# Optimization experiments

Hardware: AMD Instinct MI355X
Metric: run time of the kernel (lower is better)

The kernel has to match this reference:

```python
import math
import jax, jax.numpy as jnp
import numpy as np

GROUPS = 8

def setup_inputs() -> dict:
    key = jax.random.key(0)
    ks = jax.random.split(key, 6)
    N, H, W, C = 8, 128, 128, 512
    s = 1.0 / math.sqrt(C)
    return {
        "x": jax.random.normal(ks[0], (N, H, W, C), dtype=jnp.float32),
        "Wq": jax.random.normal(ks[1], (C, C), dtype=jnp.float32) * s,
        "Wk": jax.random.normal(ks[2], (C, C), dtype=jnp.float32) * s,
        "Wv": jax.random.normal(ks[3], (C, C), dtype=jnp.float32) * s,
        "Wo": jax.random.normal(ks[4], (C, C), dtype=jnp.float32) * s,
        "bo": jnp.zeros((C,), dtype=jnp.float32),
    }

def reference(x, Wq, Wk, Wv, Wo, bo):
    # width=False: attend along H axis -> permute to [N, W, H, C]
    x = jnp.transpose(x, (0, 2, 1, 3))
    N, W, H, C = x.shape
    g = GROUPS
    gp = C // g  # group_planes (head dim)
    xr = x.reshape(N * W, H, C)
    # torch nn.Linear: y = x @ W^T
    q = (xr @ Wq.T).reshape(N * W, H, g, gp)
    k = (xr @ Wk.T).reshape(N * W, H, g, gp)
    v = (xr @ Wv.T).reshape(N * W, H, g, gp)
    attn = jnp.einsum('nigc,njgc->nijg', q, k / math.sqrt(gp))
    attn = jax.nn.softmax(attn, axis=2)
    out = jnp.einsum('nijg,njgc->nigc', attn, v)
    out = out.reshape(N * W, H, C)
    out = out @ Wo.T + bo
    out = out.reshape(N, W, H, C)
    return jnp.transpose(out, (0, 2, 1, 3))
```

## Files before the change

kernel.cpp:

```cpp
#include <hip/hip_runtime.h>
#include <stdint.h>


#define QKV_LD 1536

typedef __attribute__((ext_vector_type(4))) float f32x4;
typedef __attribute__((ext_vector_type(8))) short bf16x8;
typedef unsigned short u16;
typedef unsigned int u32;

static __device__ __forceinline__ u16 f2bf(float f){
    union { float f; u32 u; } v; v.f = f;
    u32 r = v.u + 0x7fffu + ((v.u >> 16) & 1u);
    return (u16)(r >> 16);
}

static __device__ __forceinline__ void gload16(const void* g, void* l){
    __builtin_amdgcn_global_load_lds((const __attribute__((address_space(1))) void*)g,
                                     (__attribute__((address_space(3))) void*)l, 16, 0, 0);
}

__global__ void k_wconv(const float* __restrict__ Wq, const float* __restrict__ Wk,
                        const float* __restrict__ Wv, const float* __restrict__ Wo,
                        u16* __restrict__ Wcat, u16* __restrict__ Wob){
    int e = (blockIdx.x * 256 + threadIdx.x) * 4;
    if (e < 1536*512) {
        int row = e >> 9, col = e & 511;
        const float* s = (row < 512) ? (Wq + row*512)
                        : (row < 1024 ? Wk + (row-512)*512 : Wv + (row-1024)*512);
        float4 v = *(const float4*)(s + col);
        ushort4 o = { f2bf(v.x), f2bf(v.y), f2bf(v.z), f2bf(v.w) };
        *(ushort4*)(Wcat + e) = o;
    } else {
        int e2 = e - 1536*512;
        float4 v = *(const float4*)(Wo + e2);
        ushort4 o = { f2bf(v.x), f2bf(v.y), f2bf(v.z), f2bf(v.w) };
        *(ushort4*)(Wob + e2) = o;
    }
}

__global__ void k_xconv(const float* __restrict__ x, u16* __restrict__ xb, int n0){
    int t = blockIdx.x * 256 + threadIdx.x;
    int ml = t >> 6;
    int c0 = (t & 63) << 3;
    int nl = ml >> 7, h = ml & 127;
    int n = n0 + nl, nb = n >> 7, w = n & 127;
    const float* src = x + (size_t)((nb*128 + h)*128 + w) * 512 + c0;
    float4 a = *(const float4*)(src);
    float4 b = *(const float4*)(src + 4);
    uint4 o;
    o.x = (u32)f2bf(a.x) | ((u32)f2bf(a.y) << 16);
    o.y = (u32)f2bf(a.z) | ((u32)f2bf(a.w) << 16);
    o.z = (u32)f2bf(b.x) | ((u32)f2bf(b.y) << 16);
    o.w = (u32)f2bf(b.z) | ((u32)f2bf(b.w) << 16);
    *(uint4*)(xb + (size_t)ml*512 + c0) = o;
}

template<int LDA, int NCOL, bool OUTPROJ>
__global__ __launch_bounds__(256, 2) void k_gemm(const u16* __restrict__ A, const u16* __restrict__ B,
                                                 void* __restrict__ Cout, const float* __restrict__ bias,
                                                 int n0, int nrow){
    __shared__ char sm[32768];
    const int tid = threadIdx.x;
    const int wid = tid >> 6, lane = tid & 63, lg = lane >> 4, li = lane & 15;
    const int bid = blockIdx.x;
    const int xcd = bid & 7, l = bid >> 3;
    const int row_tile = xcd * (nrow >> 3) + l / NCOL;
    const int col_tile = l % NCOL;
    const int m0 = row_tile * 128, nn0 = col_tile * 128;
    const int wm = (wid >> 1) * 64, wn = (wid & 1) * 64;

    f32x4 acc[4][4];
    #pragma unroll
    for (int i = 0; i < 4; ++i)
        #pragma unroll
        for (int j = 0; j < 4; ++j)
            acc[i][j] = f32x4{0.f, 0.f, 0.f, 0.f};

    for (int k0 = 0; k0 < 512; k0 += 64) {
        if (k0) __syncthreads();
        #pragma unroll
        for (int it = 0; it < 4; ++it) {
            int gi = it*256 + tid;
            int row = gi >> 3, gs = gi & 7;
            int sw = (gs ^ (row & 7)) << 4;
            gload16((const char*)(A + (size_t)(m0 + row)*LDA + k0) + sw,
                    sm + it*4096 + wid*1024);
            gload16((const char*)(B + (size_t)(nn0 + row)*512 + k0) + sw,
                    sm + 16384 + it*4096 + wid*1024);
        }
        __syncthreads();
        #pragma unroll
        for (int ks = 0; ks < 2; ++ks) {
            bf16x8 af[4], bfr[4];
            #pragma unroll
            for (int t = 0; t < 4; ++t) {
                int ra = wm + t*16 + li;
                af[t]  = *(const bf16x8*)(sm + ra*128 + ((ks*64 + lg*16) ^ ((ra & 7) << 4)));
                int rb = wn + t*16 + li;
                bfr[t] = *(const bf16x8*)(sm + 16384 + rb*128 + ((ks*64 + lg*16) ^ ((rb & 7) << 4)));
            }
            #pragma unroll
            for (int i = 0; i < 4; ++i)
                #pragma unroll
                for (int j = 0; j < 4; ++j)
                    acc[i][j] = __builtin_amdgcn_mfma_f32_16x16x32_bf16(af[i], bfr[j], acc[i][j], 0, 0, 0);
        }
    }

    if (!OUTPROJ) {
        u16* C = (u16*)Cout;
        #pragma unroll
        for (int i = 0; i < 4; ++i)
            #pragma unroll
            for (int j = 0; j < 4; ++j)
                #pragma unroll
                for (int r = 0; r < 4; ++r) {
                    int row = m0 + wm + i*16 + lg*4 + r;
                    int col = nn0 + wn + j*16 + li;
                    C[(size_t)row*QKV_LD + col] = f2bf(acc[i][j][r]);
                }
    } else {
        float* C = (float*)Cout;
        #pragma unroll
        for (int i = 0; i < 4; ++i)
            #pragma unroll
            for (int j = 0; j < 4; ++j)
                #pragma unroll
                for (int r = 0; r < 4; ++r) {
                    int row = m0 + wm + i*16 + lg*4 + r;
                    int col = nn0 + wn + j*16 + li;
                    int mg = n0*128 + row;
                    int n = mg >> 7, ii = mg & 127;
                    int nb = n >> 7, w = n & 127;
                    C[(size_t)((nb*128 + ii)*128 + w) * 512 + col] = acc[i][j][r] + bias[col];
                }
    }
}

__global__ __launch_bounds__(256, 2) void k_attn(u16* __restrict__ QKV){
    __shared__ char sm[52224];
    const int g = blockIdx.x;
    const int nl = blockIdx.y;
    const int tid = threadIdx.x;
    const int wid = tid >> 6, lane = tid & 63, lg = lane >> 4, li = lane & 15;

    u16* Qg = QKV + (size_t)nl*128*QKV_LD + g*64;

    #pragma unroll
    for (int it = 0; it < 4; ++it) {
        int gi = it*256 + tid;
        int row = gi >> 3, gs = gi & 7;
        int sw = (gs ^ (row & 7)) << 4;
        gload16((const char*)(Qg + (size_t)row*QKV_LD) + sw,        sm + it*4096 + wid*1024);
        gload16((const char*)(Qg + 512 + (size_t)row*QKV_LD) + sw,  sm + 16384 + it*4096 + wid*1024);
    }
    {
        int j = tid & 127, ch = tid >> 7;
        const u16* src = Qg + 1024 + (size_t)j*QKV_LD + ch*32;
        uint4 a0 = *(const uint4*)(src);
        uint4 a1 = *(const uint4*)(src + 8);
        uint4 a2 = *(const uint4*)(src + 16);
        uint4 a3 = *(const uint4*)(src + 24);
        u32 w[16] = {a0.x,a0.y,a0.z,a0.w, a1.x,a1.y,a1.z,a1.w,
                     a2.x,a2.y,a2.z,a2.w, a3.x,a3.y,a3.z,a3.w};
        char* dst = sm + 34816 + ch*32*272 + j*2;
        #pragma unroll
        for (int cc = 0; cc < 32; ++cc) {
            u32 word = w[cc >> 1];
            u16 val = (cc & 1) ? (u16)(word >> 16) : (u16)(word & 0xffffu);
            *(u16*)(dst + cc*272) = val;
        }
    }
    __syncthreads();

    const int i0w = wid*32;
    f32x4 s[2][8];
    #pragma unroll
    for (int t = 0; t < 2; ++t)
        #pragma unroll
        for (int tj = 0; tj < 8; ++tj)
            s[t][tj] = f32x4{0.f,0.f,0.f,0.f};

    #pragma unroll
    for (int ks = 0; ks < 2; ++ks) {
        bf16x8 qf[2];
        #pragma unroll
        for (int t = 0; t < 2; ++t) {
            int ra = i0w + t*16 + li;
            qf[t] = *(const bf16x8*)(sm + ra*128 + ((ks*64 + lg*16) ^ ((ra & 7) << 4)));
        }
        #pragma unroll
        for (int tj = 0; tj < 8; ++tj) {
            int rb = tj*16 + li;
            bf16x8 kf = *(const bf16x8*)(sm + 16384 + rb*128 + ((ks*64 + lg*16) ^ ((rb & 7) << 4)));
            #pragma unroll
            for (int t = 0; t < 2; ++t)
                s[t][tj] = __builtin_amdgcn_mfma_f32_16x16x32_bf16(qf[t], kf, s[t][tj], 0, 0, 0);
        }
    }
    __syncthreads();

    char* pb = sm + wid*8704;
    #pragma unroll
    for (int t = 0; t < 2; ++t) {
        #pragma unroll
        for (int r = 0; r < 4; ++r) {
            float mx = -1e30f;
            #pragma unroll
            for (int tj = 0; tj < 8; ++tj) mx = fmaxf(mx, s[t][tj][r]);
            #pragma unroll
            for (int off = 1; off < 16; off <<= 1) mx = fmaxf(mx, __shfl_xor(mx, off, 64));
            float p[8]; float sum = 0.f;
            #pragma unroll
            for (int tj = 0; tj < 8; ++tj) { p[tj] = __expf((s[t][tj][r] - mx)*0.125f); sum += p[tj]; }
            #pragma unroll
            for (int off = 1; off < 16; off <<= 1) sum += __shfl_xor(sum, off, 64);
            float inv = 1.0f / sum;
            int prow = t*16 + lg*4 + r;
            #pragma unroll
            for (int tj = 0; tj < 8; ++tj)
                *(u16*)(pb + prow*272 + (tj*16 + li)*2) = f2bf(p[tj]*inv);
        }
    }

    f32x4 o[2][4];
    #pragma unroll
    for (int t = 0; t < 2; ++t)
        #pragma unroll
        for (int tc = 0; tc < 4; ++tc)
            o[t][tc] = f32x4{0.f,0.f,0.f,0.f};

    #pragma unroll
    for (int ks = 0; ks < 4; ++ks) {
        bf16x8 pf[2];
        #pragma unroll
        for (int t = 0; t < 2; ++t)
            pf[t] = *(const bf16x8*)(pb + (t*16 + li)*272 + (ks*64 + lg*16));
        #pragma unroll
        for (int tc = 0; tc < 4; ++tc) {
            bf16x8 vf = *(const bf16x8*)(sm + 34816 + (tc*16 + li)*272 + (ks*64 + lg*16));
            #pragma unroll
            for (int t = 0; t < 2; ++t)
                o[t][tc] = __builtin_amdgcn_mfma_f32_16x16x32_bf16(pf[t], vf, o[t][tc], 0, 0, 0);
        }
    }

    #pragma unroll
    for (int t = 0; t < 2; ++t)
        #pragma unroll
        for (int tc = 0; tc < 4; ++tc)
            #pragma unroll
            for (int r = 0; r < 4; ++r) {
                int irow = i0w + t*16 + lg*4 + r;
                int col = tc*16 + li;
                Qg[(size_t)irow*QKV_LD + col] = f2bf(o[t][tc][r]);
            }
}

extern "C" void kernel_launch(void* const* d_in, const int* in_sizes, int n_in,
                              void* d_out, int out_size, void* d_ws, size_t ws_size,
                              hipStream_t stream){
    const float* x  = (const float*)d_in[0];
    const float* Wq = (const float*)d_in[1];
    const float* Wk = (const float*)d_in[2];
    const float* Wv = (const float*)d_in[3];
    const float* Wo = (const float*)d_in[4];
    const float* bo = (const float*)d_in[5];

    char* ws = (char*)d_ws;
    u16* Wcat = (u16*)ws;
    u16* Wob  = Wcat + 1536*512;

    int CN = 1024;
    while (CN > 64 && (size_t)2097152 + (size_t)CN*524288 > ws_size) CN >>= 1;
    u16* xb  = (u16*)(ws + 2097152);
    u16* QKV = xb + (size_t)CN*128*512;

    k_wconv<<<1024, 256, 0, stream>>>(Wq, Wk, Wv, Wo, Wcat, Wob);
    int nch = 1024 / CN;
    for (int ch = 0; ch < nch; ++ch) {
        int n0 = ch * CN;
        k_xconv<<<CN*32, 256, 0, stream>>>(x, xb, n0);
        k_gemm<512,    12, false><<<CN*12, 256, 0, stream>>>(xb, Wcat, QKV, nullptr, 0, CN);
        k_attn<<<dim3(8, CN), 256, 0, stream>>>(QKV);
        k_gemm<QKV_LD, 4,  true ><<<CN*4,  256, 0, stream>>>(QKV, Wob, d_out, bo, n0, CN);
    }
}
```

Before: 663.1 us.

## Replace GEMM with 256x256-tile, 8-wave, double-buffered pipelined kernel

Swaps the 128x128 single-buffered GEMM for a 256x256 tile kernel with 8 waves, 128KB of dynamic LDS, and double-buffered global-to-LDS loads. Prefetch of the next k-slab is interleaved with MFMA phases using explicit vmcnt waits, barriers and setprio. The goal is to hide memory latency and raise data reuse per tile in both the QKV and output projections. In exchange it uses more LDS and registers and launches fewer, larger blocks, which may leave some CUs idle at tile boundaries.

Measured after the change: 626.3 us. 1.06x faster.

```diff
diff --git a/kernel.cpp b/kernel.cpp
--- a/kernel.cpp
+++ b/kernel.cpp
@@ -8,6 +8,11 @@
 typedef __attribute__((ext_vector_type(8))) short bf16x8;
 typedef unsigned short u16;
 typedef unsigned int u32;
+
+#define CBAR() asm volatile("" ::: "memory")
+#define SBAR() do { CBAR(); __builtin_amdgcn_s_barrier(); CBAR(); } while(0)
+#define LGKM0() do { asm volatile("s_waitcnt lgkmcnt(0)" ::: "memory"); __builtin_amdgcn_sched_barrier(0); } while(0)
+#define VMC(n) asm volatile("s_waitcnt vmcnt(" #n ")" ::: "memory")
 
 static __device__ __forceinline__ u16 f2bf(float f){
     union { float f; u32 u; } v; v.f = f;
@@ -57,83 +62,159 @@
 }
 
 template<int LDA, int NCOL, bool OUTPROJ>
-__global__ __launch_bounds__(256, 2) void k_gemm(const u16* __restrict__ A, const u16* __restrict__ B,
-                                                 void* __restrict__ Cout, const float* __restrict__ bias,
-                                                 int n0, int nrow){
-    __shared__ char sm[32768];
+__global__ __launch_bounds__(512, 2) void k_gemm2(const u16* __restrict__ A, const u16* __restrict__ B,
+                                                  void* __restrict__ Cout, const float* __restrict__ bias,
+                                                  int n0, int nrow){
+    extern __shared__ char smc[];
     const int tid = threadIdx.x;
     const int wid = tid >> 6, lane = tid & 63, lg = lane >> 4, li = lane & 15;
+    const int wm = wid >> 2, wn = wid & 3;
     const int bid = blockIdx.x;
     const int xcd = bid & 7, l = bid >> 3;
     const int row_tile = xcd * (nrow >> 3) + l / NCOL;
     const int col_tile = l % NCOL;
-    const int m0 = row_tile * 128, nn0 = col_tile * 128;
-    const int wm = (wid >> 1) * 64, wn = (wid & 1) * 64;
-
-    f32x4 acc[4][4];
-    #pragma unroll
-    for (int i = 0; i < 4; ++i)
+    const int m0 = row_tile * 256, nn0 = col_tile * 256;
+
+    auto stage = [&](const u16* __restrict__ G, int gbase, int kbase, int ld, char* slab){
+        #pragma unroll
+        for (int i = 0; i < 2; ++i) {
+            int R = wid*32 + i*16;
+            int r = R + (lane >> 2);
+            int srcq = (lane & 3) ^ ((r >> 1) & 3);
+            gload16((const char*)(G + (size_t)(gbase + r)*ld + kbase) + srcq*16,
+                    slab + R*64);
+        }
+    };
+
+    f32x4 acc[8][4];
+    #pragma unroll
+    for (int i = 0; i < 8; ++i)
         #pragma unroll
         for (int j = 0; j < 4; ++j)
             acc[i][j] = f32x4{0.f, 0.f, 0.f, 0.f};
 
-    for (int k0 = 0; k0 < 512; k0 += 64) {
-        if (k0) __syncthreads();
-        #pragma unroll
-        for (int it = 0; it < 4; ++it) {
-            int gi = it*256 + tid;
-            int row = gi >> 3, gs = gi & 7;
-            int sw = (gs ^ (row & 7)) << 4;
-            gload16((const char*)(A + (size_t)(m0 + row)*LDA + k0) + sw,
-                    sm + it*4096 + wid*1024);
-            gload16((const char*)(B + (size_t)(nn0 + row)*512 + k0) + sw,
-                    sm + 16384 + it*4096 + wid*1024);
-        }
-        __syncthreads();
-        #pragma unroll
-        for (int ks = 0; ks < 2; ++ks) {
-            bf16x8 af[4], bfr[4];
-            #pragma unroll
-            for (int t = 0; t < 4; ++t) {
-                int ra = wm + t*16 + li;
-                af[t]  = *(const bf16x8*)(sm + ra*128 + ((ks*64 + lg*16) ^ ((ra & 7) << 4)));
-                int rb = wn + t*16 + li;
-                bfr[t] = *(const bf16x8*)(sm + 16384 + rb*128 + ((ks*64 + lg*16) ^ ((rb & 7) << 4)));
-            }
-            #pragma unroll
-            for (int i = 0; i < 4; ++i)
-                #pragma unroll
-                for (int j = 0; j < 4; ++j)
-                    acc[i][j] = __builtin_amdgcn_mfma_f32_16x16x32_bf16(af[i], bfr[j], acc[i][j], 0, 0, 0);
-        }
+    stage(A, m0, 0,  LDA, smc + 0*16384);
+    stage(B, nn0, 0, 512, smc + 1*16384);
+    stage(A, m0, 32, LDA, smc + 2*16384);
+    stage(B, nn0, 32, 512, smc + 3*16384);
+    VMC(4);
+    SBAR();
+
+    const int nT = 8;
+    int cur = 0;
+    bf16x8 af[4], bfr[4];
+
+    for (int t = 0; t < nT; ++t) {
+        const bool pf = (t + 1 < nT);
+        char* bc = smc + cur*65536;
+        char* bn = smc + (cur^1)*65536;
+        const int kn = (t + 1) * 64;
+
+        #pragma unroll
+        for (int f = 0; f < 4; ++f) {
+            int r = wm*128 + f*16 + li;
+            af[f] = *(const bf16x8*)(bc + 0*16384 + r*64 + (((lg ^ (r>>1)) & 3) << 4));
+        }
+        #pragma unroll
+        for (int f = 0; f < 4; ++f) {
+            int r = wn*64 + f*16 + li;
+            bfr[f] = *(const bf16x8*)(bc + 1*16384 + r*64 + (((lg ^ (r>>1)) & 3) << 4));
+        }
+        if (pf) stage(A, m0, kn, LDA, bn + 0*16384);
+        SBAR(); LGKM0();
+        __builtin_amdgcn_s_setprio(1);
+        #pragma unroll
+        for (int f = 0; f < 4; ++f)
+            #pragma unroll
+            for (int n = 0; n < 4; ++n)
+                acc[f][n] = __builtin_amdgcn_mfma_f32_16x16x32_bf16(af[f], bfr[n], acc[f][n], 0, 0, 0);
+        __builtin_amdgcn_s_setprio(0);
+        SBAR();
+
+        #pragma unroll
+        for (int f = 0; f < 4; ++f) {
+            int r = wm*128 + (4+f)*16 + li;
+            af[f] = *(const bf16x8*)(bc + 0*16384 + r*64 + (((lg ^ (r>>1)) & 3) << 4));
+        }
+        if (pf) stage(B, nn0, kn, 512, bn + 1*16384);
+        if (pf) { VMC(4); } else { VMC(0); }
+        SBAR(); LGKM0();
+        __builtin_amdgcn_s_setprio(1);
+        #pragma unroll
+        for (int f = 0; f < 4; ++f)
+            #pragma unroll
+            for (int n = 0; n < 4; ++n)
+                acc[4+f][n] = __builtin_amdgcn_mfma_f32_16x16x32_bf16(af[f], bfr[n], acc[4+f][n], 0, 0, 0);
+        __builtin_amdgcn_s_setprio(0);
+        SBAR();
+
+        #pragma unroll
+        for (int f = 0; f < 4; ++f) {
+            int r = wm*128 + f*16 + li;
+            af[f] = *(const bf16x8*)(bc + 2*16384 + r*64 + (((lg ^ (r>>1)) & 3) << 4));
+        }
+        #pragma unroll
+        for (int f = 0; f < 4; ++f) {
+            int r = wn*64 + f*16 + li;
+            bfr[f] = *(const bf16x8*)(bc + 3*16384 + r*64 + (((lg ^ (r>>1)) & 3) << 4));
+        }
+        if (pf) stage(A, m0, kn + 32, LDA, bn + 2*16384);
+        SBAR(); LGKM0();
+        __builtin_amdgcn_s_setprio(1);
+        #pragma unroll
+        for (int f = 0; f < 4; ++f)
+            #pragma unroll
+            for (int n = 0; n < 4; ++n)
+                acc[f][n] = __builtin_amdgcn_mfma_f32_16x16x32_bf16(af[f], bfr[n], acc[f][n], 0, 0, 0);
+        __builtin_amdgcn_s_setprio(0);
+        SBAR();
+
+        #pragma unroll
+        for (int f = 0; f < 4; ++f) {
+            int r = wm*128 + (4+f)*16 + li;
+            af[f] = *(const bf16x8*)(bc + 2*16384 + r*64 + (((lg ^ (r>>1)) & 3) << 4));
+        }
+        if (pf) stage(B, nn0, kn + 32, 512, bn + 3*16384);
+        if (pf) { VMC(4); }
+        SBAR(); LGKM0();
+        __builtin_amdgcn_s_setprio(1);
+        #pragma unroll
+        for (int f = 0; f < 4; ++f)
+            #pragma unroll
+            for (int n = 0; n < 4; ++n)
+                acc[4+f][n] = __builtin_amdgcn_mfma_f32_16x16x32_bf16(af[f], bfr[n], acc[4+f][n], 0, 0, 0);
+        __builtin_amdgcn_s_setprio(0);
+        SBAR();
+
+        cur ^= 1;
     }
 
     if (!OUTPROJ) {
         u16* C = (u16*)Cout;
         #pragma unroll
-        for (int i = 0; i < 4; ++i)
-            #pragma unroll
-            for (int j = 0; j < 4; ++j)
+        for (int mf = 0; mf < 8; ++mf)
+            #pragma unroll
+            for (int nf = 0; nf < 4; ++nf)
                 #pragma unroll
                 for (int r = 0; r < 4; ++r) {
-                    int row = m0 + wm + i*16 + lg*4 + r;
-                    int col = nn0 + wn + j*16 + li;
-                    C[(size_t)row*QKV_LD + col] = f2bf(acc[i][j][r]);
+                    int row = m0 + wm*128 + mf*16 + lg*4 + r;
+                    int col = nn0 + wn*64 + nf*16 + li;
+                    C[(size_t)row*QKV_LD + col] = f2bf(acc[mf][nf][r]);
                 }
     } else {
         float* C = (float*)Cout;
         #pragma unroll
-        for (int i = 0; i < 4; ++i)
-            #pragma unroll
-            for (int j = 0; j < 4; ++j)
+        for (int mf = 0; mf < 8; ++mf)
+            #pragma unroll
+            for (int nf = 0; nf < 4; ++nf)
                 #pragma unroll
                 for (int r = 0; r < 4; ++r) {
-                    int row = m0 + wm + i*16 + lg*4 + r;
-                    int col = nn0 + wn + j*16 + li;
+                    int row = m0 + wm*128 + mf*16 + lg*4 + r;
+                    int col = nn0 + wn*64 + nf*16 + li;
                     int mg = n0*128 + row;
                     int n = mg >> 7, ii = mg & 127;
                     int nb = n >> 7, w = n & 127;
-                    C[(size_t)((nb*128 + ii)*128 + w) * 512 + col] = acc[i][j][r] + bias[col];
+                    C[(size_t)((nb*128 + ii)*128 + w) * 512 + col] = acc[mf][nf][r] + bias[col];
                 }
     }
 }
@@ -277,13 +358,19 @@
     u16* xb  = (u16*)(ws + 2097152);
     u16* QKV = xb + (size_t)CN*128*512;
 
+    hipFuncSetAttribute((const void*)&k_gemm2<512, 6, false>,
+                        hipFuncAttributeMaxDynamicSharedMemorySize, 131072);
+    hipFuncSetAttribute((const void*)&k_gemm2<QKV_LD, 2, true>,
+                        hipFuncAttributeMaxDynamicSharedMemorySize, 131072);
+
     k_wconv<<<1024, 256, 0, stream>>>(Wq, Wk, Wv, Wo, Wcat, Wob);
     int nch = 1024 / CN;
     for (int ch = 0; ch < nch; ++ch) {
         int n0 = ch * CN;
+        int nrow = (CN * 128) / 256;
         k_xconv<<<CN*32, 256, 0, stream>>>(x, xb, n0);
-        k_gemm<512,    12, false><<<CN*12, 256, 0, stream>>>(xb, Wcat, QKV, nullptr, 0, CN);
+        k_gemm2<512,    6, false><<<nrow*6, 512, 131072, stream>>>(xb, Wcat, QKV, nullptr, 0, nrow);
         k_attn<<<dim3(8, CN), 256, 0, stream>>>(QKV);
-        k_gemm<QKV_LD, 4,  true ><<<CN*4,  256, 0, stream>>>(QKV, Wob, d_out, bo, n0, CN);
-    }
-}
+        k_gemm2<QKV_LD, 2, true ><<<nrow*2, 512, 131072, stream>>>(QKV, Wob, d_out, bo, n0, nrow);
+    }
+}
```

## Replace GEMM with 256x128-tile, 512-thread, triple-buffered async-load pipeline

Applied to the files above, without the earlier changes.

Both projection GEMMs now use a new kernel with 8 waves and a 256x128 output tile. The K loop runs in steps of 32 with a 3-stage LDS ring filled by direct global-to-LDS loads, ordered by explicit vmcnt waits and a single barrier per step, plus setprio around the MFMA block. The aim is to overlap global loads with MFMA work and to reuse each B tile across more rows. In exchange it uses 72KB of dynamic LDS per block and drops the XOR swizzle, so the 64-byte-stride LDS reads may hit bank conflicts.

Measured after the change: 641.8 us. 1.03x faster.

```diff
diff --git a/kernel.cpp b/kernel.cpp
--- a/kernel.cpp
+++ b/kernel.cpp
@@ -8,6 +8,11 @@
 typedef __attribute__((ext_vector_type(8))) short bf16x8;
 typedef unsigned short u16;
 typedef unsigned int u32;
+
+#define CBAR() asm volatile("" ::: "memory")
+#define SBAR() do { CBAR(); __builtin_amdgcn_s_barrier(); CBAR(); } while(0)
+#define LGKM0() do { asm volatile("s_waitcnt lgkmcnt(0)" ::: "memory"); __builtin_amdgcn_sched_barrier(0); } while(0)
+#define VMC(n) asm volatile("s_waitcnt vmcnt(" #n ")" ::: "memory")
 
 static __device__ __forceinline__ u16 f2bf(float f){
     union { float f; u32 u; } v; v.f = f;
@@ -57,18 +62,30 @@
 }
 
 template<int LDA, int NCOL, bool OUTPROJ>
-__global__ __launch_bounds__(256, 2) void k_gemm(const u16* __restrict__ A, const u16* __restrict__ B,
-                                                 void* __restrict__ Cout, const float* __restrict__ bias,
-                                                 int n0, int nrow){
-    __shared__ char sm[32768];
+__global__ __launch_bounds__(512, 4) void k_gemm3(const u16* __restrict__ A, const u16* __restrict__ B,
+                                                  void* __restrict__ Cout, const float* __restrict__ bias,
+                                                  int n0, int nrow){
+    extern __shared__ char smc[];
     const int tid = threadIdx.x;
     const int wid = tid >> 6, lane = tid & 63, lg = lane >> 4, li = lane & 15;
+    const int wr = wid >> 1, wc = wid & 1;
     const int bid = blockIdx.x;
     const int xcd = bid & 7, l = bid >> 3;
     const int row_tile = xcd * (nrow >> 3) + l / NCOL;
     const int col_tile = l % NCOL;
-    const int m0 = row_tile * 128, nn0 = col_tile * 128;
-    const int wm = (wid >> 1) * 64, wn = (wid & 1) * 64;
+    const int m0 = row_tile * 256, nn0 = col_tile * 128;
+
+    auto stage = [&](int s, int kb){
+        char* sl = smc + s*24576;
+        #pragma unroll
+        for (int i = 0; i < 2; ++i) {
+            int R = wid*32 + i*16;
+            gload16((const char*)(A + (size_t)(m0 + R + (lane>>2))*LDA + kb) + (lane&3)*16,
+                    sl + R*64);
+        }
+        gload16((const char*)(B + (size_t)(nn0 + wid*16 + (lane>>2))*512 + kb) + (lane&3)*16,
+                sl + 16384 + wid*1024);
+    };
 
     f32x4 acc[4][4];
     #pragma unroll
@@ -77,63 +94,64 @@
         for (int j = 0; j < 4; ++j)
             acc[i][j] = f32x4{0.f, 0.f, 0.f, 0.f};
 
-    for (int k0 = 0; k0 < 512; k0 += 64) {
-        if (k0) __syncthreads();
-        #pragma unroll
-        for (int it = 0; it < 4; ++it) {
-            int gi = it*256 + tid;
-            int row = gi >> 3, gs = gi & 7;
-            int sw = (gs ^ (row & 7)) << 4;
-            gload16((const char*)(A + (size_t)(m0 + row)*LDA + k0) + sw,
-                    sm + it*4096 + wid*1024);
-            gload16((const char*)(B + (size_t)(nn0 + row)*512 + k0) + sw,
-                    sm + 16384 + it*4096 + wid*1024);
-        }
-        __syncthreads();
-        #pragma unroll
-        for (int ks = 0; ks < 2; ++ks) {
-            bf16x8 af[4], bfr[4];
-            #pragma unroll
-            for (int t = 0; t < 4; ++t) {
-                int ra = wm + t*16 + li;
-                af[t]  = *(const bf16x8*)(sm + ra*128 + ((ks*64 + lg*16) ^ ((ra & 7) << 4)));
-                int rb = wn + t*16 + li;
-                bfr[t] = *(const bf16x8*)(sm + 16384 + rb*128 + ((ks*64 + lg*16) ^ ((rb & 7) << 4)));
-            }
-            #pragma unroll
-            for (int i = 0; i < 4; ++i)
-                #pragma unroll
-                for (int j = 0; j < 4; ++j)
-                    acc[i][j] = __builtin_amdgcn_mfma_f32_16x16x32_bf16(af[i], bfr[j], acc[i][j], 0, 0, 0);
-        }
+    stage(0, 0);
+    stage(1, 32);
+    VMC(3);
+    SBAR();
+
+    for (int t = 0; t < 16; ++t) {
+        const int sc = t % 3;
+        char* sl = smc + sc*24576;
+
+        if (t < 14) stage((sc + 2) % 3, (t + 2) * 32);
+
+        bf16x8 af[4], bfr[4];
+        #pragma unroll
+        for (int f = 0; f < 4; ++f)
+            af[f] = *(const bf16x8*)(sl + (wr*64 + f*16 + li)*64 + (lg << 4));
+        #pragma unroll
+        for (int f = 0; f < 4; ++f)
+            bfr[f] = *(const bf16x8*)(sl + 16384 + (wc*64 + f*16 + li)*64 + (lg << 4));
+
+        LGKM0();
+        __builtin_amdgcn_s_setprio(1);
+        #pragma unroll
+        for (int fi = 0; fi < 4; ++fi)
+            #pragma unroll
+            for (int fj = 0; fj < 4; ++fj)
+                acc[fi][fj] = __builtin_amdgcn_mfma_f32_16x16x32_bf16(af[fi], bfr[fj], acc[fi][fj], 0, 0, 0);
+        __builtin_amdgcn_s_setprio(0);
+
+        if (t < 13) { VMC(3); } else { VMC(0); }
+        SBAR();
     }
 
     if (!OUTPROJ) {
         u16* C = (u16*)Cout;
         #pragma unroll
-        for (int i = 0; i < 4; ++i)
-            #pragma unroll
-            for (int j = 0; j < 4; ++j)
+        for (int fi = 0; fi < 4; ++fi)
+            #pragma unroll
+            for (int fj = 0; fj < 4; ++fj)
                 #pragma unroll
                 for (int r = 0; r < 4; ++r) {
-                    int row = m0 + wm + i*16 + lg*4 + r;
-                    int col = nn0 + wn + j*16 + li;
-                    C[(size_t)row*QKV_LD + col] = f2bf(acc[i][j][r]);
+                    int row = m0 + wr*64 + fi*16 + lg*4 + r;
+                    int col = nn0 + wc*64 + fj*16 + li;
+                    C[(size_t)row*QKV_LD + col] = f2bf(acc[fi][fj][r]);
                 }
     } else {
         float* C = (float*)Cout;
         #pragma unroll
-        for (int i = 0; i < 4; ++i)
-            #pragma unroll
-            for (int j = 0; j < 4; ++j)
+        for (int fi = 0; fi < 4; ++fi)
+            #pragma unroll
+            for (int fj = 0; fj < 4; ++fj)
                 #pragma unroll
                 for (int r = 0; r < 4; ++r) {
-                    int row = m0 + wm + i*16 + lg*4 + r;
-                    int col = nn0 + wn + j*16 + li;
+                    int row = m0 + wr*64 + fi*16 + lg*4 + r;
+                    int col = nn0 + wc*64 + fj*16 + li;
                     int mg = n0*128 + row;
                     int n = mg >> 7, ii = mg & 127;
                     int nb = n >> 7, w = n & 127;
-                    C[(size_t)((nb*128 + ii)*128 + w) * 512 + col] = acc[i][j][r] + bias[col];
+                    C[(size_t)((nb*128 + ii)*128 + w) * 512 + col] = acc[fi][fj][r] + bias[col];
                 }
     }
 }
@@ -273,17 +291,23 @@
     u16* Wob  = Wcat + 1536*512;
 
     int CN = 1024;
-    while (CN > 64 && (size_t)2097152 + (size_t)CN*524288 > ws_size) CN >>= 1;
+    while (CN > 64 && (size_t)2097152 + (size_t)CN*(131072 + 393216) > ws_size) CN >>= 1;
     u16* xb  = (u16*)(ws + 2097152);
     u16* QKV = xb + (size_t)CN*128*512;
+
+    hipFuncSetAttribute((const void*)&k_gemm3<512, 12, false>,
+                        hipFuncAttributeMaxDynamicSharedMemorySize, 73728);
+    hipFuncSetAttribute((const void*)&k_gemm3<QKV_LD, 4, true>,
+                        hipFuncAttributeMaxDynamicSharedMemorySize, 73728);
 
     k_wconv<<<1024, 256, 0, stream>>>(Wq, Wk, Wv, Wo, Wcat, Wob);
     int nch = 1024 / CN;
     for (int ch = 0; ch < nch; ++ch) {
         int n0 = ch * CN;
+        int nrow = (CN * 128) / 256;
         k_xconv<<<CN*32, 256, 0, stream>>>(x, xb, n0);
-        k_gemm<512,    12, false><<<CN*12, 256, 0, stream>>>(xb, Wcat, QKV, nullptr, 0, CN);
+        k_gemm3<512,    12, false><<<nrow*12, 512, 73728, stream>>>(xb, Wcat, QKV, nullptr, 0, nrow);
         k_attn<<<dim3(8, CN), 256, 0, stream>>>(QKV);
-        k_gemm<QKV_LD, 4,  true ><<<CN*4,  256, 0, stream>>>(QKV, Wob, d_out, bo, n0, CN);
-    }
-}
+        k_gemm3<QKV_LD, 4,  true ><<<nrow*4,  512, 73728, stream>>>(QKV, Wob, d_out, bo, n0, nrow);
+    }
+}
```
